# Optimization experiments

Measured on AMD Instinct MI355X. Metric: run time of the kernel, lower is better.

## Reference

```python
import jax, jax.numpy as jnp
import numpy as np

# Loihi neuron / simulation constants (params['neuron'], params['simulation'])
VTH_MANT = 80
V_DECAY = 128
I_DECAY = 1024
REF_DELAY = 1
WGT_EXP = 0
TAU_RHO = 1.0
SCALE_RHO = 1.0
TS = 1
THETA = float(VTH_MANT * (1 << 6))      # 5120, Loihi threshold in fixed-point units
W_SCALE = float(1 << (6 + WGT_EXP))     # 64, weight scaling into Loihi fixed point


def st_floor(x):
    """floor with straight-through gradient (Loihi integer truncation)."""
    return x + jax.lax.stop_gradient(jnp.floor(x) - x)


@jax.custom_vjp
def spike_fn(v):
    # binary spike scaled by 1/Ts, as in SLAYER-Loihi
    return (v >= THETA).astype(v.dtype) * (1.0 / TS)

def _spike_fwd(v):
    return spike_fn(v), v

def _spike_bwd(v, g):
    # SLAYER surrogate: scaleRho/(tauRho*theta) * exp(-|v - theta| / (tauRho*theta))
    pdf = (SCALE_RHO / (TAU_RHO * THETA)) * jnp.exp(-jnp.abs(v - THETA) / (TAU_RHO * THETA))
    return (g * pdf,)

spike_fn.defvjp(_spike_fwd, _spike_bwd)


def quantize_w(w, step=2.0):
    """SLAYER snn.utils.quantize(w, 2) with straight-through gradient."""
    return w + jax.lax.stop_gradient(jnp.round(w / step) * step - w)


def loihi_spikes(wsp):
    """Loihi CUBA neuron scan. wsp: [T, B, C] weighted spike input -> [T, B, C] spikes."""
    i_mul = (4096.0 - I_DECAY) / 4096.0
    v_mul = (4096.0 - V_DECAY) / 4096.0

    def step(carry, x):
        I, V, ref = carry
        I = st_floor(I * i_mul) + W_SCALE * x
        V = st_floor(V * v_mul) + I
        V = jnp.where(ref > 0, jnp.zeros_like(V), V)   # refractory hold at 0
        s = spike_fn(V)
        V = V * (1.0 - s * TS)                          # reset to 0 on spike
        ref = jnp.where(s > 0, REF_DELAY - 1, jnp.maximum(ref - 1, 0))
        return (I, V, ref), s

    B, C = wsp.shape[1], wsp.shape[2]
    init = (jnp.zeros((B, C), wsp.dtype),
            jnp.zeros((B, C), wsp.dtype),
            jnp.zeros((B, C), jnp.int32))
    _, s = jax.lax.scan(step, init, wsp)
    return s


def delay_shift(x):
    """delayShift(x, 1): shift spikes one step forward in time. x: [T, B, C]."""
    return jnp.concatenate([jnp.zeros_like(x[:1]), x[:-1]], axis=0)


def setup_inputs() -> dict:
    key = jax.random.key(0)
    k1, k2, k3 = jax.random.split(key, 3)
    B, IN, HID, OUT, T = 32, 1024, 2048, 512, 256
    spike_input = (jax.random.uniform(k1, (B, IN, T)) < 0.05).astype(jnp.float32)
    W1 = jax.random.normal(k2, (HID, IN), jnp.float32) * 8.0
    W2 = jax.random.normal(k3, (OUT, HID), jnp.float32) * 8.0
    return {"spike_input": spike_input, "W1": W1, "W2": W2}


def reference(spike_input, W1, W2):
    # spike_input: [B, IN, T] binary spikes
    x = jnp.transpose(spike_input, (2, 0, 1))          # [T, B, IN]
    w1 = quantize_w(W1)
    w2 = quantize_w(W2)
    h = jnp.einsum('tbi,hi->tbh', x, w1)               # fc1 per timestep
    s1 = delay_shift(loihi_spikes(h))                  # spikeLoihi + delayShift(1)
    o = jnp.einsum('tbh,oh->tbo', s1, w2)              # fc2 per timestep
    s2 = delay_shift(loihi_spikes(o))
    return jnp.transpose(s2, (1, 2, 0))                # [B, OUT, T]
```

## Files before the change

### kernel.cpp

```cpp
#include <hip/hip_runtime.h>

typedef unsigned char u8;
typedef signed char i8;
typedef unsigned int u32;
typedef __attribute__((ext_vector_type(4))) int i32x4;

#define AS1 __attribute__((address_space(1)))
#define AS3 __attribute__((address_space(3)))

__device__ __forceinline__ void gload_lds16(const void* g, void* l) {
    __builtin_amdgcn_global_load_lds((const AS1 void*)g, (AS3 void*)l, 16, 0, 0);
}

__global__ void prep(const float* __restrict__ X, i8* __restrict__ Xb,
                     const float4* __restrict__ W1, const float4* __restrict__ W2,
                     char4* __restrict__ W1q, char4* __restrict__ W2q) {
    const int n1v = 2048 * 1024 / 4, n2v = 512 * 2048 / 4;
    __shared__ float tile[128][33];
    int bid = blockIdx.x;
    if (bid < 3072) {
        int i = bid * 256 + threadIdx.x;
        if (i < n1v) {
            float4 w = W1[i];
            char4 q;
            q.x = (i8)(int)rintf(w.x * 0.5f);
            q.y = (i8)(int)rintf(w.y * 0.5f);
            q.z = (i8)(int)rintf(w.z * 0.5f);
            q.w = (i8)(int)rintf(w.w * 0.5f);
            W1q[i] = q;
        } else {
            int j = i - n1v;
            if (j < n2v) {
                float4 w = W2[j];
                char4 q;
                q.x = (i8)(int)rintf(w.x * 0.5f);
                q.y = (i8)(int)rintf(w.y * 0.5f);
                q.z = (i8)(int)rintf(w.z * 0.5f);
                q.w = (i8)(int)rintf(w.w * 0.5f);
                W2q[j] = q;
            }
        }
        return;
    }
    bid -= 3072;
    const int B = 32, IN = 1024, T = 256;
    const int t0 = (bid & 7) * 32, i0 = ((bid >> 3) & 7) * 128, b = bid >> 6;
    const int tx = threadIdx.x & 31, ty = threadIdx.x >> 5;
    const float* src = X + (size_t)b * IN * T;
#pragma unroll
    for (int r = 0; r < 16; ++r) {
        int i = ty + r * 8;
        tile[i][tx] = src[(size_t)(i0 + i) * T + t0 + tx];
    }
    __syncthreads();
    const int cx = threadIdx.x & 31;
    const int tl0 = threadIdx.x >> 5;
#pragma unroll
    for (int r = 0; r < 4; ++r) {
        int tl = tl0 + r * 8;
        uchar4 pk;
        pk.x = (tile[cx * 4 + 0][tl] != 0.f) ? 1 : 0;
        pk.y = (tile[cx * 4 + 1][tl] != 0.f) ? 1 : 0;
        pk.z = (tile[cx * 4 + 2][tl] != 0.f) ? 1 : 0;
        pk.w = (tile[cx * 4 + 3][tl] != 0.f) ? 1 : 0;
        *(uchar4*)&Xb[((size_t)b * T + t0 + tl) * IN + i0 + cx * 4] = pk;
    }
}

__global__ __launch_bounds__(512, 4) void gemm1_scan1(
        const i8* __restrict__ A, const i8* __restrict__ Bt,
        i8* __restrict__ S1, int K) {
    __shared__ __align__(16) i8 lds[69632];
    i8*    lA   = lds;
    i8*    lB   = lds + 32768;
    short* hT   = (short*)lds;
    u32*   bits = (u32*)(lds + 65536);

    const int nwg = gridDim.x;
    const int cpx = nwg >> 3;
    const int wg  = (blockIdx.x & 7) * cpx + (blockIdx.x >> 3);
    const int bx = wg & 15;
    const int by = wg >> 4;
    const int n0 = bx * 128;
    const int m0 = by * 256;

    const int tid  = threadIdx.x;
    const int lane = tid & 63;
    const int w    = tid >> 6;
    const int wm   = w & 3;
    const int wn   = w >> 2;
    const int l15 = lane & 15;
    const int l4  = lane >> 4;
    const int sw  = l15 & 7;

    i32x4 acc[4][4] = {};
    const int flatT = tid * 16;

    for (int k0 = 0; k0 < K; k0 += 128) {
        __syncthreads();
#pragma unroll
        for (int q = 0; q < 4; ++q) {
            int fl = q * 8192 + flatT;
            int r  = fl >> 7;
            int sc = ((fl >> 4) & 7) ^ (r & 7);
            gload_lds16(A + (size_t)(m0 + r) * K + k0 + sc * 16, &lA[fl]);
        }
#pragma unroll
        for (int q = 0; q < 2; ++q) {
            int fl = q * 8192 + flatT;
            int r  = fl >> 7;
            int sc = ((fl >> 4) & 7) ^ (r & 7);
            gload_lds16(Bt + (size_t)(n0 + r) * K + k0 + sc * 16, &lB[fl]);
        }
        __syncthreads();
#pragma unroll
        for (int kk = 0; kk < 2; ++kk) {
            i32x4 af[4], bf[4];
#pragma unroll
            for (int mf = 0; mf < 4; ++mf)
                af[mf] = *(const i32x4*)&lA[(wm * 64 + mf * 16 + l15) * 128 +
                                            ((kk * 4 + l4) ^ sw) * 16];
#pragma unroll
            for (int nf = 0; nf < 4; ++nf)
                bf[nf] = *(const i32x4*)&lB[(wn * 64 + nf * 16 + l15) * 128 +
                                            ((kk * 4 + l4) ^ sw) * 16];
#pragma unroll
            for (int mf = 0; mf < 4; ++mf)
#pragma unroll
                for (int nf = 0; nf < 4; ++nf)
                    acc[mf][nf] = __builtin_amdgcn_mfma_i32_16x16x64_i8(
                        af[mf], bf[nf], acc[mf][nf], 0, 0, 0);
        }
    }
    __syncthreads();

#pragma unroll
    for (int mf = 0; mf < 4; ++mf)
#pragma unroll
        for (int nf = 0; nf < 4; ++nf) {
            int n = wn * 64 + nf * 16 + l15;
            int c = wm * 16 + mf * 4 + l4;
            int h0 = acc[mf][nf][0] * 2, h1 = acc[mf][nf][1] * 2;
            int h2 = acc[mf][nf][2] * 2, h3 = acc[mf][nf][3] * 2;
            int2 pk;
            pk.x = (h0 & 0xffff) | (h1 << 16);
            pk.y = (h2 & 0xffff) | (h3 << 16);
            *(int2*)((char*)hT + n * 512 + ((c ^ (n & 15)) << 3)) = pk;
        }
    __syncthreads();

    {
        const int ssel = blockIdx.x & 3;
        const int w1   = 4 + ((ssel + 1) & 3);
        const int nbase = (w == ssel) ? 0 : (w == w1) ? 64 : -1;
        if (nbase >= 0) {
            const int n = nbase + lane;
            const int nx = n & 15;
            const char* hrow = (char*)hT + n * 512;
            int2 ra[4], rb[4];
#pragma unroll
            for (int q = 0; q < 4; ++q)
                ra[q] = *(const int2*)(hrow + ((q ^ nx) << 3));
            u32 bw[8] = {0, 0, 0, 0, 0, 0, 0, 0};
            float I = 0.f, V = 0.f;
#pragma unroll
            for (int p = 0; p < 16; ++p) {
                if (p < 15) {
#pragma unroll
                    for (int q = 0; q < 4; ++q) {
                        int2 v = *(const int2*)(hrow + ((((p + 1) * 4 + q) ^ nx) << 3));
                        if (p & 1) ra[q] = v; else rb[q] = v;
                    }
                }
#pragma unroll
                for (int q = 0; q < 4; ++q) {
                    int2 hh = (p & 1) ? rb[q] : ra[q];
#pragma unroll
                    for (int j = 0; j < 4; ++j) {
                        int t = p * 16 + q * 4 + j;
                        short hv = (j == 0) ? (short)hh.x
                                 : (j == 1) ? (short)(hh.x >> 16)
                                 : (j == 2) ? (short)hh.y
                                            : (short)(hh.y >> 16);
                        I = floorf(I * 0.75f) + 64.f * (float)hv;
                        V = floorf(V * 0.96875f) + I;
                        if (V >= 5120.f) { bw[t >> 5] |= (1u << (t & 31)); V = 0.f; }
                    }
                }
            }
#pragma unroll
            for (int wi = 0; wi < 8; ++wi) bits[wi * 128 + n] = bw[wi];
        }
    }
    __syncthreads();

#pragma unroll
    for (int rep = 0; rep < 16; ++rep) {
        int d   = rep * 512 + tid;
        int tt  = d >> 5;
        int ndq = d & 31;
        u32 outw = 0;
        if (tt > 0) {
            int tb = tt - 1, wi = tb >> 5, sh = tb & 31;
            outw =  ((bits[wi * 128 + ndq * 4 + 0] >> sh) & 1)
                 | (((bits[wi * 128 + ndq * 4 + 1] >> sh) & 1) << 8)
                 | (((bits[wi * 128 + ndq * 4 + 2] >> sh) & 1) << 16)
                 | (((bits[wi * 128 + ndq * 4 + 3] >> sh) & 1) << 24);
        }
        *(u32*)&S1[(size_t)(m0 + tt) * 2048 + n0 + ndq * 4] = outw;
    }
}

__global__ __launch_bounds__(512, 4) void gemm2_scan2(
        const i8* __restrict__ A, const i8* __restrict__ Bt,
        float* __restrict__ out) {
    const int K = 2048;
    __shared__ __align__(16) i8 lds[74752];
    float* hT   = (float*)lds;
    u32*   bits = (u32*)(lds + 73728);

    const int nwg = gridDim.x;
    const int cpx = nwg >> 3;
    const int wg  = (blockIdx.x & 7) * cpx + (blockIdx.x >> 3);
    const int scanw = (blockIdx.x >> 6) & 7;
    const int ox = wg & 15;
    const int by = wg >> 4;
    const int n0 = ox * 32;
    const int m0 = by * 256;

    const int tid  = threadIdx.x;
    const int lane = tid & 63;
    const int w    = tid >> 6;
    const int wmq  = w & 3;
    const int wn   = w >> 2;
    const int l15 = lane & 15;
    const int l4  = lane >> 4;
    const int sw  = l15 & 7;

    i32x4 acc[4] = {};

    auto STAGE = [&](int buf, int k0) {
        i8* lA = lds + buf * 36864;
        i8* lB = lA + 32768;
#pragma unroll
        for (int q = 0; q < 4; ++q) {
            int fl = q * 8192 + tid * 16;
            int r  = fl >> 7;
            int sc = ((fl >> 4) & 7) ^ (r & 7);
            gload_lds16(A + (size_t)(m0 + r) * K + k0 + sc * 16, &lA[fl]);
        }
        if (tid < 256) {
            int fl = tid * 16;
            int r  = fl >> 7;
            int sc = ((fl >> 4) & 7) ^ (r & 7);
            gload_lds16(Bt + (size_t)(n0 + r) * K + k0 + sc * 16, &lB[fl]);
        }
    };

    auto COMPUTE = [&](int buf) {
        const i8* lA = lds + buf * 36864;
        const i8* lB = lA + 32768;
#pragma unroll
        for (int kk = 0; kk < 2; ++kk) {
            i32x4 af[4], bf;
#pragma unroll
            for (int mf = 0; mf < 4; ++mf)
                af[mf] = *(const i32x4*)&lA[(wmq * 64 + mf * 16 + l15) * 128 +
                                            ((kk * 4 + l4) ^ sw) * 16];
            bf = *(const i32x4*)&lB[(wn * 16 + l15) * 128 + ((kk * 4 + l4) ^ sw) * 16];
#pragma unroll
            for (int mf = 0; mf < 4; ++mf)
                acc[mf] = __builtin_amdgcn_mfma_i32_16x16x64_i8(
                    af[mf], bf, acc[mf], 0, 0, 0);
        }
    };

    STAGE(0, 0);
    __syncthreads();
    int cur = 0;
    for (int k0 = 0; k0 < K; k0 += 128) {
        if (k0 + 128 < K) STAGE(cur ^ 1, k0 + 128);
        COMPUTE(cur);
        __syncthreads();
        cur ^= 1;
    }

#pragma unroll
    for (int mf = 0; mf < 4; ++mf) {
        int n = wn * 16 + l15;
        int c = wmq * 16 + mf * 4 + l4;
        float4 pk;
        pk.x = (float)(acc[mf][0] * 2);
        pk.y = (float)(acc[mf][1] * 2);
        pk.z = (float)(acc[mf][2] * 2);
        pk.w = (float)(acc[mf][3] * 2);
        *(float4*)((char*)hT + n * 1024 + ((c ^ (n & 15)) << 4)) = pk;
    }
    __syncthreads();

    if (w == scanw && lane < 32) {
        const int n = lane;
        const int nx = n & 15;
        const char* hrow = (char*)hT + n * 1024;
        float4 ra[4], rb[4];
#pragma unroll
        for (int q = 0; q < 4; ++q)
            ra[q] = *(const float4*)(hrow + ((q ^ nx) << 4));
        u32 bw[8] = {0, 0, 0, 0, 0, 0, 0, 0};
        float I = 0.f, V = 0.f;
#pragma unroll
        for (int p = 0; p < 16; ++p) {
            if (p < 15) {
#pragma unroll
                for (int q = 0; q < 4; ++q) {
                    float4 v = *(const float4*)(hrow + ((((p + 1) * 4 + q) ^ nx) << 4));
                    if (p & 1) ra[q] = v; else rb[q] = v;
                }
            }
#pragma unroll
            for (int q = 0; q < 4; ++q) {
                float4 hh = (p & 1) ? rb[q] : ra[q];
#pragma unroll
                for (int j = 0; j < 4; ++j) {
                    int t = p * 16 + q * 4 + j;
                    float hv = (j == 0) ? hh.x : (j == 1) ? hh.y
                             : (j == 2) ? hh.z : hh.w;
                    I = floorf(I * 0.75f) + 64.f * hv;
                    V = floorf(V * 0.96875f) + I;
                    if (V >= 5120.f) { bw[t >> 5] |= (1u << (t & 31)); V = 0.f; }
                }
            }
        }
#pragma unroll
        for (int wi = 0; wi < 8; ++wi) bits[wi * 32 + n] = bw[wi];
    }
    __syncthreads();

#pragma unroll
    for (int rep = 0; rep < 4; ++rep) {
        int flat = rep * 512 + tid;
        int o  = flat >> 6;
        int t4 = flat & 63;
        float4 v;
#pragma unroll
        for (int j = 0; j < 4; ++j) {
            int tt = t4 * 4 + j;
            float s = 0.f;
            if (tt > 0) {
                int tb = tt - 1;
                s = (float)((bits[(tb >> 5) * 32 + o] >> (tb & 31)) & 1);
            }
            if (j == 0) v.x = s; else if (j == 1) v.y = s;
            else if (j == 2) v.z = s; else v.w = s;
        }
        *(float4*)&out[((size_t)by * 512 + n0 + o) * 256 + t4 * 4] = v;
    }
}

extern "C" void kernel_launch(void* const* d_in, const int* in_sizes, int n_in,
                              void* d_out, int out_size, void* d_ws, size_t ws_size,
                              hipStream_t stream) {
    const int B = 32, IN = 1024, HID = 2048, OUT = 512, T = 256;
    const float* spikes = (const float*)d_in[0];
    const float* W1 = (const float*)d_in[1];
    const float* W2 = (const float*)d_in[2];
    float* out = (float*)d_out;

    char* ws = (char*)d_ws;
    size_t off = 0;
    auto alloc = [&](size_t bytes) -> void* {
        void* p = ws + off;
        off += (bytes + 255) & ~(size_t)255;
        return p;
    };
    i8* Xb  = (i8*)alloc((size_t)B * T * IN);
    i8* W1q = (i8*)alloc((size_t)HID * IN);
    i8* W2q = (i8*)alloc((size_t)OUT * HID);
    i8* S1  = (i8*)alloc((size_t)B * T * HID);

    prep<<<dim3(5120), dim3(256), 0, stream>>>(
        spikes, Xb, (const float4*)W1, (const float4*)W2,
        (char4*)W1q, (char4*)W2q);
    gemm1_scan1<<<dim3(512), dim3(512), 0, stream>>>(Xb, W1q, S1, IN);
    gemm2_scan2<<<dim3(512), dim3(512), 0, stream>>>(S1, W2q, out);
}
```

Baseline: 62.19 us.

## Widen gemm2 output tile to 64 columns and halve grid

The second GEMM+scan kernel now computes 256x64 output tiles instead of 256x32, with each wave doing 4x2 MFMA fragments and all 64 lanes of one wave running the scan. The grid shrinks from 512 to 256 workgroups, and LDS use grows with launch bounds lowered to 2 blocks per SM. This halves redundant A-tile loads from S1 across column tiles, at the cost of fewer workgroups (256 on 256 CUs), lower occupancy, and a longer serial scan per block.

```diff
diff --git a/kernel.cpp b/kernel.cpp
--- a/kernel.cpp
+++ b/kernel.cpp
@@ -211,36 +211,36 @@
     }
 }
 
-__global__ __launch_bounds__(512, 4) void gemm2_scan2(
+__global__ __launch_bounds__(512, 2) void gemm2_scan2(
         const i8* __restrict__ A, const i8* __restrict__ Bt,
         float* __restrict__ out) {
     const int K = 2048;
-    __shared__ __align__(16) i8 lds[74752];
+    __shared__ __align__(16) i8 lds[81920];
     float* hT   = (float*)lds;
-    u32*   bits = (u32*)(lds + 73728);
+    u32*   bits = (u32*)(lds + 65536);
 
     const int nwg = gridDim.x;
     const int cpx = nwg >> 3;
     const int wg  = (blockIdx.x & 7) * cpx + (blockIdx.x >> 3);
-    const int scanw = (blockIdx.x >> 6) & 7;
-    const int ox = wg & 15;
-    const int by = wg >> 4;
-    const int n0 = ox * 32;
+    const int scanw = blockIdx.x & 7;
+    const int ox = wg & 7;
+    const int by = wg >> 3;
+    const int n0 = ox * 64;
     const int m0 = by * 256;
 
     const int tid  = threadIdx.x;
     const int lane = tid & 63;
     const int w    = tid >> 6;
-    const int wmq  = w & 3;
+    const int wm   = w & 3;
     const int wn   = w >> 2;
     const int l15 = lane & 15;
     const int l4  = lane >> 4;
     const int sw  = l15 & 7;
 
-    i32x4 acc[4] = {};
+    i32x4 acc[4][2] = {};
 
     auto STAGE = [&](int buf, int k0) {
-        i8* lA = lds + buf * 36864;
+        i8* lA = lds + buf * 40960;
         i8* lB = lA + 32768;
 #pragma unroll
         for (int q = 0; q < 4; ++q) {
@@ -249,7 +249,7 @@
             int sc = ((fl >> 4) & 7) ^ (r & 7);
             gload_lds16(A + (size_t)(m0 + r) * K + k0 + sc * 16, &lA[fl]);
         }
-        if (tid < 256) {
+        {
             int fl = tid * 16;
             int r  = fl >> 7;
             int sc = ((fl >> 4) & 7) ^ (r & 7);
@@ -258,20 +258,25 @@
     };
 
     auto COMPUTE = [&](int buf) {
-        const i8* lA = lds + buf * 36864;
+        const i8* lA = lds + buf * 40960;
         const i8* lB = lA + 32768;
 #pragma unroll
         for (int kk = 0; kk < 2; ++kk) {
-            i32x4 af[4], bf;
+            i32x4 af[4], bf[2];
 #pragma unroll
             for (int mf = 0; mf < 4; ++mf)
-                af[mf] = *(const i32x4*)&lA[(wmq * 64 + mf * 16 + l15) * 128 +
+                af[mf] = *(const i32x4*)&lA[(wm * 64 + mf * 16 + l15) * 128 +
                                             ((kk * 4 + l4) ^ sw) * 16];
-            bf = *(const i32x4*)&lB[(wn * 16 + l15) * 128 + ((kk * 4 + l4) ^ sw) * 16];
+#pragma unroll
+            for (int nf = 0; nf < 2; ++nf)
+                bf[nf] = *(const i32x4*)&lB[(wn * 32 + nf * 16 + l15) * 128 +
+                                            ((kk * 4 + l4) ^ sw) * 16];
 #pragma unroll
             for (int mf = 0; mf < 4; ++mf)
-                acc[mf] = __builtin_amdgcn_mfma_i32_16x16x64_i8(
-                    af[mf], bf, acc[mf], 0, 0, 0);
+#pragma unroll
+                for (int nf = 0; nf < 2; ++nf)
+                    acc[mf][nf] = __builtin_amdgcn_mfma_i32_16x16x64_i8(
+                        af[mf], bf[nf], acc[mf][nf], 0, 0, 0);
         }
     };
 
@@ -286,19 +291,21 @@
     }
 
 #pragma unroll
-    for (int mf = 0; mf < 4; ++mf) {
-        int n = wn * 16 + l15;
-        int c = wmq * 16 + mf * 4 + l4;
-        float4 pk;
-        pk.x = (float)(acc[mf][0] * 2);
-        pk.y = (float)(acc[mf][1] * 2);
-        pk.z = (float)(acc[mf][2] * 2);
-        pk.w = (float)(acc[mf][3] * 2);
-        *(float4*)((char*)hT + n * 1024 + ((c ^ (n & 15)) << 4)) = pk;
-    }
-    __syncthreads();
-
-    if (w == scanw && lane < 32) {
+    for (int mf = 0; mf < 4; ++mf)
+#pragma unroll
+        for (int nf = 0; nf < 2; ++nf) {
+            int n = wn * 32 + nf * 16 + l15;
+            int c = wm * 16 + mf * 4 + l4;
+            float4 pk;
+            pk.x = (float)(acc[mf][nf][0] * 2);
+            pk.y = (float)(acc[mf][nf][1] * 2);
+            pk.z = (float)(acc[mf][nf][2] * 2);
+            pk.w = (float)(acc[mf][nf][3] * 2);
+            *(float4*)((char*)hT + n * 1024 + ((c ^ (n & 15)) << 4)) = pk;
+        }
+    __syncthreads();
+
+    if (w == scanw) {
         const int n = lane;
         const int nx = n & 15;
         const char* hrow = (char*)hT + n * 1024;
@@ -332,12 +339,12 @@
             }
         }
 #pragma unroll
-        for (int wi = 0; wi < 8; ++wi) bits[wi * 32 + n] = bw[wi];
-    }
-    __syncthreads();
-
-#pragma unroll
-    for (int rep = 0; rep < 4; ++rep) {
+        for (int wi = 0; wi < 8; ++wi) bits[wi * 64 + n] = bw[wi];
+    }
+    __syncthreads();
+
+#pragma unroll
+    for (int rep = 0; rep < 8; ++rep) {
         int flat = rep * 512 + tid;
         int o  = flat >> 6;
         int t4 = flat & 63;
@@ -348,7 +355,7 @@
             float s = 0.f;
             if (tt > 0) {
                 int tb = tt - 1;
-                s = (float)((bits[(tb >> 5) * 32 + o] >> (tb & 31)) & 1);
+                s = (float)((bits[(tb >> 5) * 64 + o] >> (tb & 31)) & 1);
             }
             if (j == 0) v.x = s; else if (j == 1) v.y = s;
             else if (j == 2) v.z = s; else v.w = s;
@@ -382,5 +389,5 @@
         spikes, Xb, (const float4*)W1, (const float4*)W2,
         (char4*)W1q, (char4*)W2q);
     gemm1_scan1<<<dim3(512), dim3(512), 0, stream>>>(Xb, W1q, S1, IN);
-    gemm2_scan2<<<dim3(512), dim3(512), 0, stream>>>(S1, W2q, out);
-}
+    gemm2_scan2<<<dim3(256), dim3(512), 0, stream>>>(S1, W2q, out);
+}
```

New measurement: 62.16 us (median of 2 runs). No clear change (-0.0%).
